# Kernel tuning notes

Hardware: AMD Instinct MI355X
Metric: run time of the kernel (lower is better)

The kernel has to match this reference:

```python
import jax, jax.numpy as jnp
import numpy as np

N_NODES = 100000
N_EDGES = 3200000


def gcn_conv(x, edge_index, W, b, num_nodes):
    # PyG GCNConv: linear transform, add self-loops, symmetric degree norm, scatter-add, bias
    h = x @ W  # [N, out]
    src = jnp.concatenate([edge_index[0], jnp.arange(num_nodes)])  # self-loops
    dst = jnp.concatenate([edge_index[1], jnp.arange(num_nodes)])
    deg = jax.ops.segment_sum(jnp.ones_like(dst, dtype=h.dtype), dst, num_segments=num_nodes)
    dinv = jnp.where(deg > 0, jax.lax.rsqrt(deg), 0.0)
    norm = dinv[src] * dinv[dst]  # [E+N]
    msg = h[src] * norm[:, None]  # gather + scale
    out = jax.ops.segment_sum(msg, dst, num_segments=num_nodes)  # scatter-add
    return out + b


def setup_inputs() -> dict:
    key = jax.random.key(0)
    k1, k2, k3, k4 = jax.random.split(key, 4)
    x = jax.random.normal(k1, (N_NODES, 18), dtype=jnp.float32)
    edge_index = jax.random.randint(k2, (2, N_EDGES), 0, N_NODES, dtype=jnp.int64)
    W1 = jax.random.normal(k3, (18, 64), dtype=jnp.float32) * (1.0 / np.sqrt(18))
    b1 = jnp.zeros((64,), dtype=jnp.float32)
    W2 = jax.random.normal(k4, (64, 32), dtype=jnp.float32) * (1.0 / np.sqrt(64))
    b2 = jnp.zeros((32,), dtype=jnp.float32)
    return {"x": x, "edge_index": edge_index, "W1": W1, "b1": b1, "W2": W2, "b2": b2}


def reference(x, edge_index, W1, b1, W2, b2):
    h = jax.nn.relu(gcn_conv(x, edge_index, W1, b1, N_NODES))
    return gcn_conv(h, edge_index, W2, b2, N_NODES)
```

## Files before the change

kernel.cpp:

```cpp
#include <hip/hip_runtime.h>
#include <hip/hip_fp16.h>

#define F0 18
#define F1 64
#define F2 32
#define BSHIFT 8
#define BNODES 256
#define CHUNK 2048
#define CAP 9216

__global__ __launch_bounds__(256) void scatter32_kernel(const int* __restrict__ ei,
                                                        int* __restrict__ bcur,
                                                        unsigned int* __restrict__ stage,
                                                        int E, int NB) {
    __shared__ int lh[512];
    __shared__ int lb[512];
    int t = threadIdx.x;
    for (int i = t; i < NB; i += 256) lh[i] = 0;
    __syncthreads();
    int e0 = blockIdx.x * CHUNK, e1 = min(e0 + CHUNK, E);
    for (int e = e0 + t; e < e1; e += 256)
        atomicAdd(&lh[ei[E + e] >> BSHIFT], 1);
    __syncthreads();
    for (int i = t; i < NB; i += 256) {
        int c = lh[i];
        lb[i] = c ? atomicAdd(&bcur[i], c) : 0;
        lh[i] = 0;
    }
    __syncthreads();
    for (int e = e0 + t; e < e1; e += 256) {
        int s = ei[e], d = ei[E + e];
        int b = d >> BSHIFT;
        int off = lb[b] + atomicAdd(&lh[b], 1);
        if (off < CAP)
            stage[(size_t)b * CAP + off] = ((unsigned)(d & 255) << 24) | (unsigned)s;
    }
}

__global__ __launch_bounds__(512) void bucketfill_kernel(const unsigned int* __restrict__ stage,
                                                         const int* __restrict__ bcur,
                                                         int* __restrict__ rps,
                                                         int* __restrict__ rpe,
                                                         float* __restrict__ dinv,
                                                         int* __restrict__ csr,
                                                         const float* __restrict__ x,
                                                         __half* __restrict__ xp, int n) {
    __shared__ int lcnt[BNODES];
    __shared__ int lofs[BNODES];
    __shared__ float ldv[BNODES];
    int b = blockIdx.x;
    int base = b << BSHIFT;
    int nn = min(BNODES, n - base);
    int ecnt = min(bcur[b], CAP);
    int estart = b * CAP;
    int t = threadIdx.x;

    if (t < BNODES) lcnt[t] = 0;
    __syncthreads();
    for (int e = estart + t; e < estart + ecnt; e += 512)
        atomicAdd(&lcnt[stage[e] >> 24], 1);
    __syncthreads();

    int v = 0;
    if (t < BNODES) { v = (t < nn) ? lcnt[t] : 0; lofs[t] = v; }
    __syncthreads();
    for (int off = 1; off < BNODES; off <<= 1) {
        int xv = 0;
        if (t < BNODES && t >= off) xv = lofs[t - off];
        __syncthreads();
        if (t < BNODES) lofs[t] += xv;
        __syncthreads();
    }
    if (t < nn) {
        float dv = rsqrtf((float)(v + 1));
        rps[base + t] = estart + lofs[t] - v;
        rpe[base + t] = estart + lofs[t];
        dinv[base + t] = dv;
        ldv[t] = dv;
    }
    __syncthreads();
    if (t < BNODES) lcnt[t] = lofs[t] - v;
    __syncthreads();

    for (int e = estart + t; e < estart + ecnt; e += 512) {
        unsigned int pk = stage[e];
        int d = pk >> 24;
        int pos = atomicAdd(&lcnt[d], 1);
        csr[estart + pos] = (int)(pk & 0xffffffu);
    }
    for (int idx = t; idx < nn * 32; idx += 512) {
        int lv = idx >> 5, j = idx & 31;
        float val = (j < F0) ? ldv[lv] * x[(size_t)(base + lv) * F0 + j] : 0.f;
        xp[(size_t)(base + lv) * 32 + j] = __float2half(val);
    }
}

struct __align__(8) h4v { __half2 a, b; };

__global__ __launch_bounds__(256) void agg32h_kernel(const __half* __restrict__ tab,
                                                     const int* __restrict__ csr,
                                                     const int* __restrict__ rps,
                                                     const int* __restrict__ rpe,
                                                     const float* __restrict__ dinv,
                                                     const float* __restrict__ bias,
                                                     float* __restrict__ outp, int n) {
    int wid = (blockIdx.x * 256 + threadIdx.x) >> 6;
    int lane = threadIdx.x & 63;
    if (wid >= n) return;
    int sub = lane >> 3;
    int q = (lane & 7) << 2;
    int beg = rps[wid], end = rpe[wid];
    float4 acc = make_float4(0.f, 0.f, 0.f, 0.f);
    if (sub == 0) {
        h4v sv = *(const h4v*)&tab[(size_t)wid * 32 + q];
        float2 f0 = __half22float2(sv.a), f1 = __half22float2(sv.b);
        acc.x = f0.x; acc.y = f0.y; acc.z = f1.x; acc.w = f1.y;
    }
    int e = beg + sub;
    for (; e + 8 < end; e += 16) {
        int s0 = csr[e], s1 = csr[e + 8];
        h4v v0 = *(const h4v*)&tab[(size_t)s0 * 32 + q];
        h4v v1 = *(const h4v*)&tab[(size_t)s1 * 32 + q];
        float2 a0 = __half22float2(v0.a), b0 = __half22float2(v0.b);
        float2 a1 = __half22float2(v1.a), b1 = __half22float2(v1.b);
        acc.x += a0.x + a1.x; acc.y += a0.y + a1.y;
        acc.z += b0.x + b1.x; acc.w += b0.y + b1.y;
    }
    for (; e < end; e += 8) {
        int s0 = csr[e];
        h4v v0 = *(const h4v*)&tab[(size_t)s0 * 32 + q];
        float2 a0 = __half22float2(v0.a), b0 = __half22float2(v0.b);
        acc.x += a0.x; acc.y += a0.y; acc.z += b0.x; acc.w += b0.y;
    }
    for (int off = 8; off < 64; off <<= 1) {
        acc.x += __shfl_xor(acc.x, off, 64);
        acc.y += __shfl_xor(acc.y, off, 64);
        acc.z += __shfl_xor(acc.z, off, 64);
        acc.w += __shfl_xor(acc.w, off, 64);
    }
    if (sub == 0) {
        float dv = dinv[wid];
        float4 r;
        r.x = acc.x * dv; r.y = acc.y * dv; r.z = acc.z * dv; r.w = acc.w * dv;
        if (bias) { r.x += bias[q]; r.y += bias[q + 1]; r.z += bias[q + 2]; r.w += bias[q + 3]; }
        *(float4*)&outp[(size_t)wid * 32 + q] = r;
    }
}

__global__ __launch_bounds__(256) void gemm_fused_kernel(const float* __restrict__ ax,
                                                         const float* __restrict__ W1,
                                                         const float* __restrict__ b1,
                                                         const float* __restrict__ W2,
                                                         const float* __restrict__ dinv,
                                                         __half* __restrict__ h2p, int n) {
    __shared__ float W1s[F0 * F1];
    __shared__ float W2s[F1 * F2];
    __shared__ float hid[8][F1];
    __shared__ float axs[8][32];
    int t = threadIdx.x;
    for (int i = t; i < F0 * F1; i += 256) W1s[i] = W1[i];
    for (int i = t; i < F1 * F2; i += 256) W2s[i] = W2[i];
    int lv = t >> 5, j = t & 31;
    int v = blockIdx.x * 8 + lv;
    if (v < n) axs[lv][j] = ax[(size_t)v * 32 + j];
    __syncthreads();
    float h0 = b1[j], h1 = b1[j + 32];
#pragma unroll
    for (int k = 0; k < F0; ++k) {
        float a = axs[lv][k];
        h0 += a * W1s[k * F1 + j];
        h1 += a * W1s[k * F1 + j + 32];
    }
    hid[lv][j] = fmaxf(h0, 0.f);
    hid[lv][j + 32] = fmaxf(h1, 0.f);
    __syncthreads();
    float acc = 0.f;
#pragma unroll
    for (int k = 0; k < F1; ++k) acc += hid[lv][k] * W2s[k * F2 + j];
    if (v < n) h2p[(size_t)v * 32 + j] = __float2half(acc * dinv[v]);
}


extern "C" void kernel_launch(void* const* d_in, const int* in_sizes, int n_in,
                              void* d_out, int out_size, void* d_ws, size_t ws_size,
                              hipStream_t stream) {
    const float* x  = (const float*)d_in[0];
    const int*   ei = (const int*)d_in[1];
    const float* W1 = (const float*)d_in[2];
    const float* b1 = (const float*)d_in[3];
    const float* W2 = (const float*)d_in[4];
    const float* b2 = (const float*)d_in[5];
    float* out = (float*)d_out;

    int n = in_sizes[0] / F0;
    int E = in_sizes[1] / 2;
    int NB = (n + BNODES - 1) >> BSHIFT;

    char* ws = (char*)d_ws;
    size_t o = 0;
    auto alloc = [&](size_t bytes) {
        char* p = ws + o;
        o = (o + bytes + 255) & ~(size_t)255;
        return p;
    };
    int*   rps   = (int*)alloc((size_t)n * 4);
    int*   rpe   = (int*)alloc((size_t)n * 4);
    float* dinv  = (float*)alloc((size_t)n * 4);
    int*   bcur  = (int*)alloc(512 * 4);
    int*   csr   = (int*)alloc((size_t)NB * CAP * 4);
    unsigned int* stage = (unsigned int*)alloc((size_t)NB * CAP * 4);
    float* ax    = (float*)alloc((size_t)n * 32 * 4);
    __half* xp   = (__half*)alloc((size_t)n * 32 * 2);
    __half* h2p  = (__half*)stage;
    (void)ws_size; (void)n_in; (void)out_size;

    int nchunks = (E + CHUNK - 1) / CHUNK;

    hipMemsetAsync(bcur, 0, 512 * 4, stream);
    scatter32_kernel<<<nchunks, 256, 0, stream>>>(ei, bcur, stage, E, NB);
    bucketfill_kernel<<<NB, 512, 0, stream>>>(stage, bcur, rps, rpe, dinv, csr, x, xp, n);

    agg32h_kernel<<<(n + 3) / 4, 256, 0, stream>>>(xp, csr, rps, rpe, dinv, nullptr, ax, n);
    gemm_fused_kernel<<<(n + 7) / 8, 256, 0, stream>>>(ax, W1, b1, W2, dinv, h2p, n);
    agg32h_kernel<<<(n + 3) / 4, 256, 0, stream>>>(h2p, csr, rps, rpe, dinv, b2, out, n);
}
```

Baseline: 250.8 us.

## Stripe bucket counters across blocks and stage bucket edges in shared memory

Splits each destination bucket's global atomic counter into eight stripes chosen by block index, which spreads contention on the bucket-offset atomics in the scatter kernel. The bucketfill kernel gathers the per-stripe segments into a 40KB shared buffer and does both counting passes from shared memory instead of reading global stage twice. The costs are higher LDS use, which lowers occupancy, and a tighter per-stripe capacity (1280) that could overflow and silently drop edges if stripes are unbalanced. It also assumes NB*NSTRIPE fits in the scaled allocation of h2p aliasing stage.

```diff
diff --git a/kernel.cpp b/kernel.cpp
--- a/kernel.cpp
+++ b/kernel.cpp
@@ -7,7 +7,9 @@
 #define BSHIFT 8
 #define BNODES 256
 #define CHUNK 2048
-#define CAP 9216
+#define NSTRIPE 8
+#define CAPS 1280
+#define CAPB (CAPS * NSTRIPE)
 
 __global__ __launch_bounds__(256) void scatter32_kernel(const int* __restrict__ ei,
                                                         int* __restrict__ bcur,
@@ -16,6 +18,7 @@
     __shared__ int lh[512];
     __shared__ int lb[512];
     int t = threadIdx.x;
+    int s = blockIdx.x & (NSTRIPE - 1);
     for (int i = t; i < NB; i += 256) lh[i] = 0;
     __syncthreads();
     int e0 = blockIdx.x * CHUNK, e1 = min(e0 + CHUNK, E);
@@ -24,16 +27,17 @@
     __syncthreads();
     for (int i = t; i < NB; i += 256) {
         int c = lh[i];
-        lb[i] = c ? atomicAdd(&bcur[i], c) : 0;
+        lb[i] = c ? atomicAdd(&bcur[i * NSTRIPE + s], c) : 0;
         lh[i] = 0;
     }
     __syncthreads();
     for (int e = e0 + t; e < e1; e += 256) {
-        int s = ei[e], d = ei[E + e];
+        int sN = ei[e], d = ei[E + e];
         int b = d >> BSHIFT;
         int off = lb[b] + atomicAdd(&lh[b], 1);
-        if (off < CAP)
-            stage[(size_t)b * CAP + off] = ((unsigned)(d & 255) << 24) | (unsigned)s;
+        if (off < CAPS)
+            stage[(size_t)(b * NSTRIPE + s) * CAPS + off] =
+                ((unsigned)(d & 255) << 24) | (unsigned)sN;
     }
 }
 
@@ -45,20 +49,38 @@
                                                          int* __restrict__ csr,
                                                          const float* __restrict__ x,
                                                          __half* __restrict__ xp, int n) {
+    __shared__ unsigned int sbuf[CAPB];
     __shared__ int lcnt[BNODES];
     __shared__ int lofs[BNODES];
     __shared__ float ldv[BNODES];
+    __shared__ int segofs[NSTRIPE + 1];
     int b = blockIdx.x;
     int base = b << BSHIFT;
     int nn = min(BNODES, n - base);
-    int ecnt = min(bcur[b], CAP);
-    int estart = b * CAP;
+    int estart = b * CAPB;
     int t = threadIdx.x;
 
+    if (t == 0) {
+        int acc = 0;
+        for (int s = 0; s < NSTRIPE; ++s) {
+            segofs[s] = acc;
+            acc += min(bcur[b * NSTRIPE + s], CAPS);
+        }
+        segofs[NSTRIPE] = acc;
+    }
     if (t < BNODES) lcnt[t] = 0;
     __syncthreads();
-    for (int e = estart + t; e < estart + ecnt; e += 512)
-        atomicAdd(&lcnt[stage[e] >> 24], 1);
+    int ecnt = segofs[NSTRIPE];
+
+    for (int s = 0; s < NSTRIPE; ++s) {
+        int so = segofs[s], cs = segofs[s + 1] - so;
+        const unsigned int* src = stage + (size_t)(b * NSTRIPE + s) * CAPS;
+        for (int i = t; i < cs; i += 512) sbuf[so + i] = src[i];
+    }
+    __syncthreads();
+
+    for (int e = t; e < ecnt; e += 512)
+        atomicAdd(&lcnt[sbuf[e] >> 24], 1);
     __syncthreads();
 
     int v = 0;
@@ -82,8 +104,8 @@
     if (t < BNODES) lcnt[t] = lofs[t] - v;
     __syncthreads();
 
-    for (int e = estart + t; e < estart + ecnt; e += 512) {
-        unsigned int pk = stage[e];
+    for (int e = t; e < ecnt; e += 512) {
+        unsigned int pk = sbuf[e];
         int d = pk >> 24;
         int pos = atomicAdd(&lcnt[d], 1);
         csr[estart + pos] = (int)(pk & 0xffffffu);
@@ -206,9 +228,9 @@
     int*   rps   = (int*)alloc((size_t)n * 4);
     int*   rpe   = (int*)alloc((size_t)n * 4);
     float* dinv  = (float*)alloc((size_t)n * 4);
-    int*   bcur  = (int*)alloc(512 * 4);
-    int*   csr   = (int*)alloc((size_t)NB * CAP * 4);
-    unsigned int* stage = (unsigned int*)alloc((size_t)NB * CAP * 4);
+    int*   bcur  = (int*)alloc((size_t)NB * NSTRIPE * 4);
+    int*   csr   = (int*)alloc((size_t)NB * CAPB * 4);
+    unsigned int* stage = (unsigned int*)alloc((size_t)NB * CAPB * 4);
     float* ax    = (float*)alloc((size_t)n * 32 * 4);
     __half* xp   = (__half*)alloc((size_t)n * 32 * 2);
     __half* h2p  = (__half*)stage;
@@ -216,7 +238,7 @@
 
     int nchunks = (E + CHUNK - 1) / CHUNK;
 
-    hipMemsetAsync(bcur, 0, 512 * 4, stream);
+    hipMemsetAsync(bcur, 0, (size_t)NB * NSTRIPE * 4, stream);
     scatter32_kernel<<<nchunks, 256, 0, stream>>>(ei, bcur, stage, E, NB);
     bucketfill_kernel<<<NB, 512, 0, stream>>>(stage, bcur, rps, rpe, dinv, csr, x, xp, n);
 
```

Result: no change. 250.9 us (+0.0%).
